# Performance work log

Hardware: AMD Instinct MI355X
Metric: run time of the kernel (lower is better)

Reference implementation:

```python
import jax, jax.numpy as jnp
import numpy as np

K = 11      # kernel_size
PAD = 5     # (dilation*(K-1)+1 - 1)//2 with dilation=1


def _unfold(x, k, pad):
    # torch nn.Unfold ordering: channel slowest, then (ki, kj) fastest.
    B, C, H, W = x.shape
    xp = jnp.pad(x, ((0, 0), (0, 0), (pad, pad), (pad, pad)))
    # [B, C, k*k, H, W] -- small fixed loop over the 121 kernel offsets
    cols = jnp.stack([xp[:, :, i:i + H, j:j + W]
                      for i in range(k) for j in range(k)], axis=2)
    return cols.reshape(B, C * k * k, H * W)  # [B, 363, L]


def setup_inputs() -> dict:
    key = jax.random.key(0)
    ks = jax.random.split(key, 4)
    x = jax.random.normal(ks[0], (1, 3, 400, 400), dtype=jnp.float32)
    W1 = jax.random.normal(ks[1], (363, 128), dtype=jnp.float32) * 0.05
    b1 = jnp.zeros((128,), dtype=jnp.float32)
    W2 = jax.random.normal(ks[2], (128, 64), dtype=jnp.float32) * 0.08
    b2 = jnp.zeros((64,), dtype=jnp.float32)
    W3 = jax.random.normal(ks[3], (64, 8), dtype=jnp.float32) * 0.1
    b3 = jnp.zeros((8,), dtype=jnp.float32)
    return {"x": x, "W1": W1, "b1": b1, "W2": W2, "b2": b2, "W3": W3, "b3": b3}


def reference(x, W1, b1, W2, b2, W3, b3):
    B, C, H, W = x.shape
    cols = _unfold(x, K, PAD)                 # [B, 363, H*W]
    h = cols.transpose(0, 2, 1)               # [B, L, 363]
    h = jax.nn.leaky_relu(h @ W1 + b1)        # [B, L, 128], slope 0.01 = torch default
    h = jax.nn.leaky_relu(h @ W2 + b2)        # [B, L, 64]
    h = h @ W3 + b3                           # [B, L, 8]
    # Fold(kernel=1) is a reshape; squeeze(0) + permute -> [H, W, E]
    y = h[0].reshape(H, W, -1)
    # F.normalize(p=2, dim=-1, eps=1e-12)
    n = jnp.maximum(jnp.linalg.norm(y, axis=-1, keepdims=True), 1e-12)
    return y / n
```

## Files before the change

### kernel.cpp

```cpp
#include <hip/hip_runtime.h>
#include <hip/hip_bf16.h>
#include <math.h>

typedef _Float16 f16x8 __attribute__((ext_vector_type(8)));
typedef _Float16 f16x4 __attribute__((ext_vector_type(4)));
typedef float    f32x4 __attribute__((ext_vector_type(4)));

#define IMG   400
#define NPIX  160000
#define NKT1  18
#define W1P   (NKT1*8*64*8)
#define W2P   (4*4*64*8)
#define W3P   (2*64*8)
#define HSS   40
#define XPH   1938

__device__ __forceinline__ void async_cp16(const _Float16* g, _Float16* l) {
    __builtin_amdgcn_global_load_lds(
        (const __attribute__((address_space(1))) uint32_t*)g,
        (__attribute__((address_space(3))) uint32_t*)l, 16, 0, 0);
}

__global__ void pack_weights(const float* __restrict__ W1,
                             const float* __restrict__ W2,
                             const float* __restrict__ W3,
                             _Float16* __restrict__ ws)
{
    int i = blockIdx.x * blockDim.x + threadIdx.x;
    if (i < 576 * 128) {
        int kp = i >> 7, n = i & 127;
        int kt = kp >> 5, kl = kp & 31, q = kl >> 3, j = kl & 7;
        int pair = kp >> 4, kj = kp & 15;
        int c = pair / 12, ki = pair % 12;
        int mt = n >> 4, n15 = n & 15;
        int lane = q * 16 + n15;
        float v = (ki < 11 && kj < 11) ? W1[(c * 121 + ki * 11 + kj) * 128 + n] : 0.0f;
        ws[((kt * 8 + mt) * 64 + lane) * 8 + j] = (_Float16)v;
    } else if (i < 576 * 128 + 128 * 64) {
        int e = i - 576 * 128;
        int kp = e >> 6, n = e & 63;
        int kt = kp >> 5, kl = kp & 31, q = kl >> 3, j = kl & 7;
        int mt = n >> 4, n15 = n & 15;
        int lane = q * 16 + n15;
        ws[W1P + ((kt * 4 + mt) * 64 + lane) * 8 + j] = (_Float16)W2[kp * 64 + n];
    } else if (i < 576 * 128 + 128 * 64 + 64 * 16) {
        int e = i - 576 * 128 - 128 * 64;
        int kp = e >> 4, n = e & 15;
        int kt = kp >> 5, kl = kp & 31, q = kl >> 3, j = kl & 7;
        int lane = q * 16 + n;
        float v = (n < 8) ? W3[kp * 8 + n] : 0.0f;
        ws[W1P + W2P + (kt * 64 + lane) * 8 + j] = (_Float16)v;
    }
}

__global__ __launch_bounds__(128, 2) void fused_unfold_mlp(
    const float* __restrict__ x,
    const float* __restrict__ b1,
    const float* __restrict__ b2,
    const float* __restrict__ b3,
    const _Float16* __restrict__ wpack,
    float* __restrict__ out)
{
    __shared__ __align__(16) _Float16 xs[2 * XPH];
    __shared__ __align__(16) _Float16 w1s[2 * 4096];
    __shared__ __align__(16) _Float16 hs[2][64 * HSS];

    const int tid  = threadIdx.x;
    const int wave = tid >> 6;
    const int lane = tid & 63;
    const int q    = lane >> 4;
    const int n15  = lane & 15;
    const int bx   = blockIdx.x;
    const int by   = blockIdx.y;

    const _Float16* w1p = wpack;
    const _Float16* w2p = wpack + W1P;
    const _Float16* w3p = wpack + W1P + W2P;

    const int kt0 = (bx + by * 25) % NKT1;

    {
        int seg = wave * 4;
#pragma unroll
        for (int s = 0; s < 4; ++s)
            async_cp16(w1p + kt0 * 4096 + (seg + s) * 512 + lane * 8,
                       &w1s[(seg + s) * 512]);
    }

    for (int w = tid; w < 3 * 19 * 35; w += 128) {
        int col = w % 35;
        int rc  = w / 35;
        int row = rc % 19, c = rc / 19;
        int gy = by * 8 + row - 5;
        int gx = bx * 16 + col - 6;
        float v = 0.0f;
        if ((unsigned)gy < (unsigned)IMG && (unsigned)gx < (unsigned)IMG)
            v = x[c * NPIX + gy * IMG + gx];
        _Float16 hv = (_Float16)v;
        int base = (c * 19 + row) * 34;
        if (col >= 1)  xs[base + col - 1] = hv;
        if (col <= 33) xs[XPH + base + col] = hv;
    }
    __syncthreads();

    const uint32_t* xsd = (const uint32_t*)xs;
    const int h = q >> 1;
    const int u = n15 + (n15 & 1) + ((q & 1) << 3);
    const int bdw0 = (n15 & 1) * (XPH / 2) + (u >> 1);
    int bdwt[4];
#pragma unroll
    for (int t = 0; t < 4; ++t)
        bdwt[t] = bdw0 + (wave * 4 + t + h) * 17;

    f32x4 acc1[4][8];
#pragma unroll
    for (int t = 0; t < 4; ++t)
#pragma unroll
        for (int mt = 0; mt < 8; ++mt)
            acc1[t][mt] = (f32x4){0.f, 0.f, 0.f, 0.f};

    int kt = kt0;
    for (int kk = 0; kk < NKT1; ++kk) {
        if (kk) __syncthreads();
        const int buf  = kk & 1;
        const int nbuf = buf ^ 1;
        const int ktn  = (kt + 1 == NKT1) ? 0 : kt + 1;
        if (kk < NKT1 - 1) {
            int seg = wave * 4;
#pragma unroll
            for (int s = 0; s < 4; ++s)
                async_cp16(w1p + ktn * 4096 + (seg + s) * 512 + lane * 8,
                           &w1s[nbuf * 4096 + (seg + s) * 512]);
        }

        const int d6  = (kt >= 12) ? 2 : (kt >= 6 ? 1 : 0);
        const int m6  = kt - d6 * 6;
        const int rim = (d6 * 19 + 2 * m6) * 17;

        f16x8 bf[4];
#pragma unroll
        for (int t = 0; t < 4; ++t) {
            union { uint32_t u[4]; f16x8 f; } cv;
#pragma unroll
            for (int m = 0; m < 4; ++m)
                cv.u[m] = xsd[bdwt[t] + rim + m];
            bf[t] = cv.f;
        }
        const _Float16* wb = &w1s[buf * 4096];
#pragma unroll
        for (int mt = 0; mt < 8; ++mt) {
            f16x8 af = *(const f16x8*)(wb + (mt * 64 + lane) * 8);
#pragma unroll
            for (int t = 0; t < 4; ++t)
                acc1[t][mt] = __builtin_amdgcn_mfma_f32_16x16x32_f16(af, bf[t], acc1[t][mt], 0, 0, 0);
        }
        kt = ktn;
    }

    _Float16* hw = hs[wave];

    f32x4 acc2[4][4];
#pragma unroll
    for (int t = 0; t < 4; ++t)
#pragma unroll
        for (int mt = 0; mt < 4; ++mt)
            acc2[t][mt] = (f32x4){0.f, 0.f, 0.f, 0.f};

#pragma unroll
    for (int k2 = 0; k2 < 4; ++k2) {
#pragma unroll
        for (int lm = 0; lm < 2; ++lm) {
            int mt = 2 * k2 + lm;
            float4 bb = *(const float4*)(b1 + mt * 16 + q * 4);
#pragma unroll
            for (int t = 0; t < 4; ++t) {
                f16x4 hv;
#pragma unroll
                for (int r = 0; r < 4; ++r) {
                    float v = acc1[t][mt][r] + ((const float*)&bb)[r];
                    v = fmaxf(v, 0.01f * v);
                    hv[r] = (_Float16)v;
                }
                *(f16x4*)(hw + (t * 16 + n15) * HSS + lm * 16 + q * 4) = hv;
            }
        }
        f16x8 bf[4];
#pragma unroll
        for (int t = 0; t < 4; ++t)
            bf[t] = *(const f16x8*)(hw + (t * 16 + n15) * HSS + q * 8);
#pragma unroll
        for (int mt2 = 0; mt2 < 4; ++mt2) {
            f16x8 af = *(const f16x8*)(w2p + ((k2 * 4 + mt2) * 64 + lane) * 8);
#pragma unroll
            for (int t = 0; t < 4; ++t)
                acc2[t][mt2] = __builtin_amdgcn_mfma_f32_16x16x32_f16(af, bf[t], acc2[t][mt2], 0, 0, 0);
        }
    }

    f16x8 af3[2];
#pragma unroll
    for (int k3 = 0; k3 < 2; ++k3)
        af3[k3] = *(const f16x8*)(w3p + (k3 * 64 + lane) * 8);

    f32x4 acc3[4];
#pragma unroll
    for (int t = 0; t < 4; ++t)
        acc3[t] = (f32x4){0.f, 0.f, 0.f, 0.f};
#pragma unroll
    for (int k3 = 0; k3 < 2; ++k3) {
#pragma unroll
        for (int lm = 0; lm < 2; ++lm) {
            int mt2 = 2 * k3 + lm;
            float4 bb = *(const float4*)(b2 + mt2 * 16 + q * 4);
#pragma unroll
            for (int t = 0; t < 4; ++t) {
                f16x4 hv;
#pragma unroll
                for (int r = 0; r < 4; ++r) {
                    float v = acc2[t][mt2][r] + ((const float*)&bb)[r];
                    v = fmaxf(v, 0.01f * v);
                    hv[r] = (_Float16)v;
                }
                *(f16x4*)(hw + (t * 16 + n15) * HSS + lm * 16 + q * 4) = hv;
            }
        }
#pragma unroll
        for (int t = 0; t < 4; ++t) {
            f16x8 bf = *(const f16x8*)(hw + (t * 16 + n15) * HSS + q * 8);
            acc3[t] = __builtin_amdgcn_mfma_f32_16x16x32_f16(af3[k3], bf, acc3[t], 0, 0, 0);
        }
    }

    float4 bb3 = make_float4(0.f, 0.f, 0.f, 0.f);
    if (q < 2) bb3 = *(const float4*)(b3 + q * 4);
#pragma unroll
    for (int t = 0; t < 4; ++t) {
        float v0 = acc3[t][0] + bb3.x;
        float v1 = acc3[t][1] + bb3.y;
        float v2 = acc3[t][2] + bb3.z;
        float v3 = acc3[t][3] + bb3.w;
        float s = v0 * v0 + v1 * v1 + v2 * v2 + v3 * v3;
        s += __shfl_xor(s, 16);
        s += __shfl_xor(s, 32);
        float inv = 1.0f / fmaxf(sqrtf(s), 1e-12f);
        if (q < 2) {
            int p = (by * 8 + wave * 4 + t) * IMG + bx * 16 + n15;
            float4 o = make_float4(v0 * inv, v1 * inv, v2 * inv, v3 * inv);
            *(float4*)(out + p * 8 + q * 4) = o;
        }
    }
}

extern "C" void kernel_launch(void* const* d_in, const int* in_sizes, int n_in,
                              void* d_out, int out_size, void* d_ws, size_t ws_size,
                              hipStream_t stream) {
    const float* x  = (const float*)d_in[0];
    const float* W1 = (const float*)d_in[1];
    const float* b1 = (const float*)d_in[2];
    const float* W2 = (const float*)d_in[3];
    const float* b2 = (const float*)d_in[4];
    const float* W3 = (const float*)d_in[5];
    const float* b3 = (const float*)d_in[6];
    float* out = (float*)d_out;
    _Float16* ws = (_Float16*)d_ws;

    pack_weights<<<dim3(324), dim3(256), 0, stream>>>(W1, W2, W3, ws);
    fused_unfold_mlp<<<dim3(25, 50), dim3(128), 0, stream>>>(x, b1, b2, b3, ws, out);
}
```

Baseline: 109.7 us.

## Split output channels across four waves and load W1 fragments directly into registers

The block grows to four waves, each owning half the output channels for four pixel rows. This halves per-wave accumulators and raises occupancy. The W1 LDS double buffer with async copies is replaced by register double-buffered global loads, which removes the per-k-step barrier. Layer activations now go through a shared block-wide LDS buffer with barriers between layers. The cost is more global/L2 weight traffic per block plus extra syncthreads in the epilogue.

```diff
diff --git a/kernel.cpp b/kernel.cpp
--- a/kernel.cpp
+++ b/kernel.cpp
@@ -12,14 +12,9 @@
 #define W1P   (NKT1*8*64*8)
 #define W2P   (4*4*64*8)
 #define W3P   (2*64*8)
-#define HSS   40
+#define H1S   136
+#define H2S   72
 #define XPH   1938
-
-__device__ __forceinline__ void async_cp16(const _Float16* g, _Float16* l) {
-    __builtin_amdgcn_global_load_lds(
-        (const __attribute__((address_space(1))) uint32_t*)g,
-        (__attribute__((address_space(3))) uint32_t*)l, 16, 0, 0);
-}
 
 __global__ void pack_weights(const float* __restrict__ W1,
                              const float* __restrict__ W2,
@@ -53,7 +48,7 @@
     }
 }
 
-__global__ __launch_bounds__(128, 2) void fused_unfold_mlp(
+__global__ __launch_bounds__(256, 3) void fused_unfold_mlp(
     const float* __restrict__ x,
     const float* __restrict__ b1,
     const float* __restrict__ b2,
@@ -62,14 +57,15 @@
     float* __restrict__ out)
 {
     __shared__ __align__(16) _Float16 xs[2 * XPH];
-    __shared__ __align__(16) _Float16 w1s[2 * 4096];
-    __shared__ __align__(16) _Float16 hs[2][64 * HSS];
+    __shared__ __align__(16) _Float16 hb[128 * H1S];
 
     const int tid  = threadIdx.x;
     const int wave = tid >> 6;
     const int lane = tid & 63;
     const int q    = lane >> 4;
     const int n15  = lane & 15;
+    const int och  = wave & 1;
+    const int rh   = wave >> 1;
     const int bx   = blockIdx.x;
     const int by   = blockIdx.y;
 
@@ -79,15 +75,12 @@
 
     const int kt0 = (bx + by * 25) % NKT1;
 
-    {
-        int seg = wave * 4;
-#pragma unroll
-        for (int s = 0; s < 4; ++s)
-            async_cp16(w1p + kt0 * 4096 + (seg + s) * 512 + lane * 8,
-                       &w1s[(seg + s) * 512]);
-    }
-
-    for (int w = tid; w < 3 * 19 * 35; w += 128) {
+    f16x8 afA[4], afB[4];
+#pragma unroll
+    for (int m2 = 0; m2 < 4; ++m2)
+        afA[m2] = *(const f16x8*)(w1p + ((kt0 * 8 + och * 4 + m2) * 64 + lane) * 8);
+
+    for (int w = tid; w < 3 * 19 * 35; w += 256) {
         int col = w % 35;
         int rc  = w / 35;
         int row = rc % 19, c = rc / 19;
@@ -110,27 +103,25 @@
     int bdwt[4];
 #pragma unroll
     for (int t = 0; t < 4; ++t)
-        bdwt[t] = bdw0 + (wave * 4 + t + h) * 17;
-
-    f32x4 acc1[4][8];
+        bdwt[t] = bdw0 + (rh * 4 + t + h) * 17;
+
+    f32x4 acc1[4][4];
 #pragma unroll
     for (int t = 0; t < 4; ++t)
 #pragma unroll
-        for (int mt = 0; mt < 8; ++mt)
-            acc1[t][mt] = (f32x4){0.f, 0.f, 0.f, 0.f};
-
-    int kt = kt0;
+        for (int m2 = 0; m2 < 4; ++m2)
+            acc1[t][m2] = (f32x4){0.f, 0.f, 0.f, 0.f};
+
+    int kt  = kt0;
+    int ktn = (kt0 + 1 == NKT1) ? 0 : kt0 + 1;
+#pragma unroll
     for (int kk = 0; kk < NKT1; ++kk) {
-        if (kk) __syncthreads();
-        const int buf  = kk & 1;
-        const int nbuf = buf ^ 1;
-        const int ktn  = (kt + 1 == NKT1) ? 0 : kt + 1;
+        f16x8* cur = (kk & 1) ? afB : afA;
+        f16x8* nxt = (kk & 1) ? afA : afB;
         if (kk < NKT1 - 1) {
-            int seg = wave * 4;
-#pragma unroll
-            for (int s = 0; s < 4; ++s)
-                async_cp16(w1p + ktn * 4096 + (seg + s) * 512 + lane * 8,
-                           &w1s[nbuf * 4096 + (seg + s) * 512]);
+#pragma unroll
+            for (int m2 = 0; m2 < 4; ++m2)
+                nxt[m2] = *(const f16x8*)(w1p + ((ktn * 8 + och * 4 + m2) * 64 + lane) * 8);
         }
 
         const int d6  = (kt >= 12) ? 2 : (kt >= 6 ? 1 : 0);
@@ -146,105 +137,109 @@
                 cv.u[m] = xsd[bdwt[t] + rim + m];
             bf[t] = cv.f;
         }
-        const _Float16* wb = &w1s[buf * 4096];
-#pragma unroll
-        for (int mt = 0; mt < 8; ++mt) {
-            f16x8 af = *(const f16x8*)(wb + (mt * 64 + lane) * 8);
+#pragma unroll
+        for (int m2 = 0; m2 < 4; ++m2)
 #pragma unroll
             for (int t = 0; t < 4; ++t)
-                acc1[t][mt] = __builtin_amdgcn_mfma_f32_16x16x32_f16(af, bf[t], acc1[t][mt], 0, 0, 0);
-        }
-        kt = ktn;
-    }
-
-    _Float16* hw = hs[wave];
-
-    f32x4 acc2[4][4];
+                acc1[t][m2] = __builtin_amdgcn_mfma_f32_16x16x32_f16(cur[m2], bf[t], acc1[t][m2], 0, 0, 0);
+
+        kt  = ktn;
+        ktn = (ktn + 1 == NKT1) ? 0 : ktn + 1;
+    }
+
+#pragma unroll
+    for (int m2 = 0; m2 < 4; ++m2) {
+        float4 bb = *(const float4*)(b1 + och * 64 + m2 * 16 + q * 4);
+#pragma unroll
+        for (int t = 0; t < 4; ++t) {
+            f16x4 hv;
+#pragma unroll
+            for (int r = 0; r < 4; ++r) {
+                float v = acc1[t][m2][r] + ((const float*)&bb)[r];
+                v = fmaxf(v, 0.01f * v);
+                hv[r] = (_Float16)v;
+            }
+            int px = (rh * 4 + t) * 16 + n15;
+            *(f16x4*)(hb + px * H1S + och * 64 + m2 * 16 + q * 4) = hv;
+        }
+    }
+    __syncthreads();
+
+    f32x4 acc2[4][2];
 #pragma unroll
     for (int t = 0; t < 4; ++t)
 #pragma unroll
-        for (int mt = 0; mt < 4; ++mt)
-            acc2[t][mt] = (f32x4){0.f, 0.f, 0.f, 0.f};
+        for (int m = 0; m < 2; ++m)
+            acc2[t][m] = (f32x4){0.f, 0.f, 0.f, 0.f};
 
 #pragma unroll
     for (int k2 = 0; k2 < 4; ++k2) {
-#pragma unroll
-        for (int lm = 0; lm < 2; ++lm) {
-            int mt = 2 * k2 + lm;
-            float4 bb = *(const float4*)(b1 + mt * 16 + q * 4);
-#pragma unroll
-            for (int t = 0; t < 4; ++t) {
-                f16x4 hv;
-#pragma unroll
-                for (int r = 0; r < 4; ++r) {
-                    float v = acc1[t][mt][r] + ((const float*)&bb)[r];
-                    v = fmaxf(v, 0.01f * v);
-                    hv[r] = (_Float16)v;
-                }
-                *(f16x4*)(hw + (t * 16 + n15) * HSS + lm * 16 + q * 4) = hv;
+        f16x8 bf2[4];
+#pragma unroll
+        for (int t = 0; t < 4; ++t) {
+            int px = (rh * 4 + t) * 16 + n15;
+            bf2[t] = *(const f16x8*)(hb + px * H1S + k2 * 32 + q * 8);
+        }
+#pragma unroll
+        for (int m = 0; m < 2; ++m) {
+            f16x8 af = *(const f16x8*)(w2p + ((k2 * 4 + och * 2 + m) * 64 + lane) * 8);
+#pragma unroll
+            for (int t = 0; t < 4; ++t)
+                acc2[t][m] = __builtin_amdgcn_mfma_f32_16x16x32_f16(af, bf2[t], acc2[t][m], 0, 0, 0);
+        }
+    }
+    __syncthreads();
+
+#pragma unroll
+    for (int m = 0; m < 2; ++m) {
+        float4 bb = *(const float4*)(b2 + och * 32 + m * 16 + q * 4);
+#pragma unroll
+        for (int t = 0; t < 4; ++t) {
+            f16x4 hv;
+#pragma unroll
+            for (int r = 0; r < 4; ++r) {
+                float v = acc2[t][m][r] + ((const float*)&bb)[r];
+                v = fmaxf(v, 0.01f * v);
+                hv[r] = (_Float16)v;
             }
-        }
-        f16x8 bf[4];
-#pragma unroll
-        for (int t = 0; t < 4; ++t)
-            bf[t] = *(const f16x8*)(hw + (t * 16 + n15) * HSS + q * 8);
-#pragma unroll
-        for (int mt2 = 0; mt2 < 4; ++mt2) {
-            f16x8 af = *(const f16x8*)(w2p + ((k2 * 4 + mt2) * 64 + lane) * 8);
-#pragma unroll
-            for (int t = 0; t < 4; ++t)
-                acc2[t][mt2] = __builtin_amdgcn_mfma_f32_16x16x32_f16(af, bf[t], acc2[t][mt2], 0, 0, 0);
-        }
-    }
+            int px = (rh * 4 + t) * 16 + n15;
+            *(f16x4*)(hb + px * H2S + och * 32 + m * 16 + q * 4) = hv;
+        }
+    }
+    __syncthreads();
 
     f16x8 af3[2];
 #pragma unroll
     for (int k3 = 0; k3 < 2; ++k3)
         af3[k3] = *(const f16x8*)(w3p + (k3 * 64 + lane) * 8);
 
-    f32x4 acc3[4];
-#pragma unroll
-    for (int t = 0; t < 4; ++t)
-        acc3[t] = (f32x4){0.f, 0.f, 0.f, 0.f};
+    f32x4 acc3[2];
+    acc3[0] = (f32x4){0.f, 0.f, 0.f, 0.f};
+    acc3[1] = (f32x4){0.f, 0.f, 0.f, 0.f};
 #pragma unroll
     for (int k3 = 0; k3 < 2; ++k3) {
 #pragma unroll
-        for (int lm = 0; lm < 2; ++lm) {
-            int mt2 = 2 * k3 + lm;
-            float4 bb = *(const float4*)(b2 + mt2 * 16 + q * 4);
-#pragma unroll
-            for (int t = 0; t < 4; ++t) {
-                f16x4 hv;
-#pragma unroll
-                for (int r = 0; r < 4; ++r) {
-                    float v = acc2[t][mt2][r] + ((const float*)&bb)[r];
-                    v = fmaxf(v, 0.01f * v);
-                    hv[r] = (_Float16)v;
-                }
-                *(f16x4*)(hw + (t * 16 + n15) * HSS + lm * 16 + q * 4) = hv;
-            }
-        }
-#pragma unroll
-        for (int t = 0; t < 4; ++t) {
-            f16x8 bf = *(const f16x8*)(hw + (t * 16 + n15) * HSS + q * 8);
-            acc3[t] = __builtin_amdgcn_mfma_f32_16x16x32_f16(af3[k3], bf, acc3[t], 0, 0, 0);
+        for (int tt = 0; tt < 2; ++tt) {
+            int px = (2 * wave + tt) * 16 + n15;
+            f16x8 bf = *(const f16x8*)(hb + px * H2S + k3 * 32 + q * 8);
+            acc3[tt] = __builtin_amdgcn_mfma_f32_16x16x32_f16(af3[k3], bf, acc3[tt], 0, 0, 0);
         }
     }
 
     float4 bb3 = make_float4(0.f, 0.f, 0.f, 0.f);
     if (q < 2) bb3 = *(const float4*)(b3 + q * 4);
 #pragma unroll
-    for (int t = 0; t < 4; ++t) {
-        float v0 = acc3[t][0] + bb3.x;
-        float v1 = acc3[t][1] + bb3.y;
-        float v2 = acc3[t][2] + bb3.z;
-        float v3 = acc3[t][3] + bb3.w;
+    for (int tt = 0; tt < 2; ++tt) {
+        float v0 = acc3[tt][0] + bb3.x;
+        float v1 = acc3[tt][1] + bb3.y;
+        float v2 = acc3[tt][2] + bb3.z;
+        float v3 = acc3[tt][3] + bb3.w;
         float s = v0 * v0 + v1 * v1 + v2 * v2 + v3 * v3;
         s += __shfl_xor(s, 16);
         s += __shfl_xor(s, 32);
         float inv = 1.0f / fmaxf(sqrtf(s), 1e-12f);
         if (q < 2) {
-            int p = (by * 8 + wave * 4 + t) * IMG + bx * 16 + n15;
+            int p = (by * 8 + 2 * wave + tt) * IMG + bx * 16 + n15;
             float4 o = make_float4(v0 * inv, v1 * inv, v2 * inv, v3 * inv);
             *(float4*)(out + p * 8 + q * 4) = o;
         }
@@ -265,5 +260,5 @@
     _Float16* ws = (_Float16*)d_ws;
 
     pack_weights<<<dim3(324), dim3(256), 0, stream>>>(W1, W2, W3, ws);
-    fused_unfold_mlp<<<dim3(25, 50), dim3(128), 0, stream>>>(x, b1, b2, b3, ws, out);
+    fused_unfold_mlp<<<dim3(25, 50), dim3(256), 0, stream>>>(x, b1, b2, b3, ws, out);
 }
```

Result: faster. 98.61 us (-10.1%).
